# Optimization experiments

Hardware: AMD Instinct MI355X
Metric: run time of the kernel (lower is better)

The kernel has to match this reference:

```python
import jax, jax.numpy as jnp
import numpy as np

NUM_SLOTS = 50
NUM_TAGS = 1 + 2 * NUM_SLOTS  # 'O' + B-/I- per slot = 101
BATCH = 256
SEQ_LEN = 2048


def _build_type_indices():
    # Replicates CRF.build_transitions index construction for a BIO label vocab.
    labels = ['O'] + [p + f's{i}' for i in range(NUM_SLOTS) for p in ('B-', 'I-')]
    m1 = {'O': 0, 'B': 1, 'I': 2}
    m2 = {'O': 0, 'B': 3, 'I': 4}
    t0 = np.zeros((NUM_TAGS, NUM_TAGS), dtype=np.int64)
    t1 = np.zeros((NUM_TAGS, NUM_TAGS), dtype=np.int64)
    for i, li in enumerate(labels):
        for j, lj in enumerate(labels):
            if li != 'O' and li[2:] != lj[2:]:
                t0[i, j], t1[i, j] = m1[li[0]], m2[lj[0]]
            else:
                t0[i, j], t1[i, j] = m1[li[0]], m1[lj[0]]
    return jnp.asarray(t0), jnp.asarray(t1)


def setup_inputs() -> dict:
    key = jax.random.key(0)
    k1, k2, k3, k4, k5, k6 = jax.random.split(key, 6)
    feats = jax.random.normal(k1, (BATCH, SEQ_LEN, NUM_TAGS), dtype=jnp.float32)
    # cdt_transitions is log of the fixed prior table in the original module
    cdt = jnp.log(jnp.array([[0.6, 0.4, 0.001, 0.001, 0.001],
                             [0.3, 0.1, 0.1, 0.5, 0.001],
                             [0.6, 0.1, 0.1, 0.2, 0.001]], dtype=jnp.float32))
    start_transitions = jax.random.normal(k2, (NUM_TAGS,), dtype=jnp.float32)
    stop_transitions = jax.random.normal(k3, (NUM_TAGS,), dtype=jnp.float32)
    # random valid lengths in [S/2, S]; mask[:, :len] = 1
    lengths = jax.random.randint(k4, (BATCH,), SEQ_LEN // 2, SEQ_LEN + 1)
    mask = (jnp.arange(SEQ_LEN)[None, :] < lengths[:, None]).astype(jnp.int32)
    tags = jax.random.randint(k5, (BATCH, SEQ_LEN), 0, NUM_TAGS)
    types0, types1 = _build_type_indices()
    return {
        'feats': feats,
        'cdt_transitions': cdt,
        'start_transitions': start_transitions,
        'stop_transitions': stop_transitions,
        'mask': mask,
        'tags': tags,
        'types0': types0,
        'types1': types1,
    }


def reference(feats, cdt_transitions, start_transitions, stop_transitions,
              mask, tags, types0, types1):
    # build_transitions: gather (num_tags, num_tags) log-transition matrix
    trans = cdt_transitions[types0, types1]  # (T, T)
    B, S, T = feats.shape
    maskb = mask.astype(bool)

    # ---- forward algorithm (log partition) via lax.scan over time ----
    feats_t = jnp.swapaxes(feats, 0, 1)   # (S, B, T)
    mask_t = jnp.swapaxes(maskb, 0, 1)    # (S, B)
    partition0 = feats_t[0] + start_transitions[None, :]  # (B, T)

    def step(partition, xs):
        f, mk = xs  # f: (B, T), mk: (B,)
        # cur_values[b, i, j] = f[b, j] + partition[b, i] + trans[i, j]
        cur = f[:, None, :] + partition[:, :, None] + trans[None, :, :]
        cur_partition = jax.nn.logsumexp(cur, axis=1)  # (B, T)
        new_partition = jnp.where(mk[:, None], cur_partition, partition)
        return new_partition, None

    partition, _ = jax.lax.scan(step, partition0, (feats_t[1:], mask_t[1:]))
    forward_score = jax.nn.logsumexp(partition + stop_transitions[None, :], axis=1)  # (B,)

    # ---- gold path score ----
    mf = maskb.astype(feats.dtype)
    feat_score = jnp.sum(
        jnp.take_along_axis(feats, tags[..., None], axis=2)[..., 0] * mf, axis=1)
    trans_score = jnp.sum(trans[tags[:, :-1], tags[:, 1:]] * mf[:, 1:], axis=1)
    start_score = start_transitions[tags[:, 0]]
    lengths = jnp.sum(mask, axis=1).astype(jnp.int32)  # (B,)
    end_ids = jnp.take_along_axis(tags, (lengths - 1)[:, None], axis=1)[:, 0]
    stop_score = stop_transitions[end_ids]
    gold_score = feat_score + start_score + trans_score + stop_score

    return forward_score - gold_score  # (B,) negative log-likelihood per sequence
```

## Files before the change

kernel.cpp:

```cpp
#include <hip/hip_runtime.h>
#include <math.h>

#define NSLOTS 50
#define T 101
#define SEQ 2048
#define CHUNK 16

template<int CTRL>
__device__ __forceinline__ float dpp_xadd(float v) {
    int x = __builtin_amdgcn_update_dpp(0, __float_as_int(v), CTRL, 0xF, 0xF, true);
    return v + __int_as_float(x);
}

__device__ __forceinline__ float wsum64(float v) {
    v = dpp_xadd<0xB1>(v);
    v = dpp_xadd<0x4E>(v);
    v = dpp_xadd<0x141>(v);
    v = dpp_xadd<0x140>(v);
    v = dpp_xadd<0x142>(v);
    v = dpp_xadd<0x143>(v);
    int s = __builtin_amdgcn_readlane(__float_as_int(v), 63);
    return __int_as_float(s);
}

__device__ __forceinline__ void gl_lds(const float* g, float* lds) {
#if __has_builtin(__builtin_amdgcn_global_load_lds)
    __builtin_amdgcn_global_load_lds((const __attribute__((address_space(1))) void*)g,
        (__attribute__((address_space(3))) void*)lds, 4, 0, 0);
#else
    lds[threadIdx.x & 63] = *g;
#endif
}

__global__ __launch_bounds__(192, 1) void crf_nll_kernel(
    const float* __restrict__ feats,
    const float* __restrict__ cdt,
    const float* __restrict__ start_t,
    const float* __restrict__ stop_t,
    const int*   __restrict__ mask,
    const int*   __restrict__ tags,
    float*       __restrict__ out)
{
    const int b = blockIdx.x, tid = threadIdx.x;
    const int wave = tid >> 6, l = tid & 63;
    const float* fb = feats + (size_t)b * SEQ * T;
    const int*   mb = mask + (size_t)b * SEQ;
    const int*   tb = tags + (size_t)b * SEQ;

    __shared__ float S[64 * 128];
    __shared__ float res[2];

    float mc = 0.f;
    for (int t = l; t < SEQ; t += 64) mc += (float)mb[t];
    const int len    = (int)(wsum64(mc) + 0.5f);
    const int nsteps = len - 1;
    const int nper   = (nsteps + CHUNK - 1) / CHUNK;
    const int nfull  = nsteps / CHUNK;

    const float actm = (l < NSLOTS) ? 1.f : 0.f;
    const int aB = (2*l+1 <= 100) ? 2*l+1 : 100;
    const int aI = (2*l+2 <= 100) ? 2*l+2 : 100;
    const int s1 = (2*l+1 <= 100) ? 2*l+1 : 0;
    const int s2 = (2*l+2 <= 100) ? 2*l+2 : 0;

    const float pOO=__expf(cdt[0]),  pOB=__expf(cdt[1]),  pOI=__expf(cdt[2]);
    const float pBO=__expf(cdt[5]),  pBBs=__expf(cdt[6]), pBIs=__expf(cdt[7]),
                pBBd=__expf(cdt[8]), pBId=__expf(cdt[9]);
    const float pIO=__expf(cdt[10]), pIBs=__expf(cdt[11]), pIIs=__expf(cdt[12]),
                pIBd=__expf(cdt[13]), pIId=__expf(cdt[14]);
    const float dBB=pBBs-pBBd, dIB=pIBs-pIBd, dBI=pBIs-pBId, dII=pIIs-pIId;

    float xB=0.f, xI=0.f, xO=1.f, accF=0.f, uB=0.f, uI=0.f, pOOxO=pOO;
    int accE = 0;
    float f0B=0,f0I=0,f0O=0,f1B=0,f1I=0,f1O=0;
    float gs = 0.f;

    if (wave == 1) {
        #pragma unroll
        for (int k = 0; k < 2*CHUNK; ++k) {
            const float* row = fb + (size_t)(1 + k) * T;
            float* dst = &S[(size_t)k * 128];
            gl_lds(row + s1, dst);
            gl_lds(row + s2, dst + 64);
        }
    } else if (wave == 0) {
        float pO0 = fb[0] + start_t[0];
        xB = actm * __expf(fb[aB] + start_t[aB] - pO0);
        xI = actm * __expf(fb[aI] + start_t[aI] - pO0);
        accF = pO0;
        uB = __builtin_fmaf(xB, dBB, __builtin_fmaf(xI, dIB, pOB));
        uI = __builtin_fmaf(xB, dBI, __builtin_fmaf(xI, dII, pOI));
    } else {
        if (l == 0) {
            int tg0 = tb[0];
            gs = fb[tg0] + start_t[tg0];
        }
    }
    __syncthreads();

    if (wave == 0) {
        f0B = S[l];       f0I = S[64 + l];       f0O = S[50];
        f1B = S[128 + l]; f1I = S[128 + 64 + l]; f1O = S[128 + 50];
    }

#define STEP_BODY(GUARDED)                                                     \
    {                                                                          \
        const int t  = 1 + p * CHUNK + k;                                      \
        const int w2 = ((t + 1) & 63) << 7;              \
        float nB = S[w2 + l], nI = S[w2 + 64 + l], nO = S[w2 + 50];            \
        if (!(GUARDED) || t <= nsteps) {                                       \
            float gB = actm * __expf(f0B - f0O);                \
            float gI = actm * __expf(f0I - f0O);                               \
            int   ke = ((__float_as_int(xO) >> 23) & 0xFF) - 127;              \
            float r  = __int_as_float((127 - ke) << 23);     \
            accE += ke;                                                        \
            float XB = wsum64(xB);                                             \
            float XI = wsum64(xI);                                             \
            float NOr = __builtin_fmaf(XI,pIO, __builtin_fmaf(XB,pBO, pOOxO));  \
            float NB  = gB * __builtin_fmaf(XI,pIBd, __builtin_fmaf(XB,pBBd, uB)); \
            float NI  = gI * __builtin_fmaf(XI,pIId, __builtin_fmaf(XB,pBId, uI)); \
            xB = NB * r; xI = NI * r; xO = NOr * r;                            \
            pOOxO = pOO * xO;                          \
            uB = __builtin_fmaf(xB, dBB, __builtin_fmaf(xI, dIB, pOB * xO));   \
            uI = __builtin_fmaf(xB, dBI, __builtin_fmaf(xI, dII, pOI * xO));   \
            accF += f0O;                                                       \
        }                                                                      \
        f0B=f1B; f0I=f1I; f0O=f1O; f1B=nB; f1I=nI; f1O=nO;                     \
    }

    for (int p = 0; p < nper; ++p) {
        if (wave == 0) {
            if (p < nfull) {
                #pragma unroll
                for (int k = 0; k < CHUNK; ++k) STEP_BODY(false)
            } else {
                #pragma unroll
                for (int k = 0; k < CHUNK; ++k) STEP_BODY(true)
            }
        } else if (wave == 1) {
            const int ci = p + 2;
            #pragma unroll
            for (int k = 0; k < CHUNK; ++k) {
                int t = 1 + ci * CHUNK + k;
                t = (t < SEQ) ? t : (SEQ - 1);
                const float* row = fb + (size_t)t * T;
                float* dst = &S[(size_t)((ci * CHUNK + k) & 63) * 128];
                gl_lds(row + s1, dst);
                gl_lds(row + s2, dst + 64);
            }
        } else {
            if (p >= 1 && l < CHUNK) {
                int t = 1 + (p - 1) * CHUNK + l;
                if (t <= nsteps) {
                    int tg = tb[t], tp = tb[t - 1];
                    int c1 = (tp == 0) ? 0 : ((tp & 1) ? 1 : 2);
                    int c2 = (tg == 0) ? 0 : ((tg & 1) ? 1 : 2);
                    int si = (tp - 1) >> 1, sj = (tg - 1) >> 1;
                    int t1 = (tp != 0 && si != sj) ? ((c2 == 0) ? 0 : c2 + 2) : c2;
                    gs += cdt[c1 * 5 + t1];
                    int idx = (tg == 0) ? 50 : ((tg & 1) ? ((tg - 1) >> 1) : (64 + ((tg - 2) >> 1)));
                    gs += S[(((t - 1) & 63) << 7) + idx];
                }
            }
        }
        __syncthreads();
    }
#undef STEP_BODY

    if (wave == 0) {
        float W = actm * (xB * __expf(stop_t[aB]) + xI * __expf(stop_t[aI]));
        float tot = wsum64(W) + xO * __expf(stop_t[0]);
        float fwd = accF + 0.69314718055994530942f * (float)accE + __logf(tot);
        if (l == 0) res[0] = fwd;
    } else if (wave == 2) {
        if (l < CHUNK) {
            int t = 1 + (nper - 1) * CHUNK + l;
            if (t >= 1 && t <= nsteps) {
                int tg = tb[t], tp = tb[t - 1];
                int c1 = (tp == 0) ? 0 : ((tp & 1) ? 1 : 2);
                int c2 = (tg == 0) ? 0 : ((tg & 1) ? 1 : 2);
                int si = (tp - 1) >> 1, sj = (tg - 1) >> 1;
                int t1 = (tp != 0 && si != sj) ? ((c2 == 0) ? 0 : c2 + 2) : c2;
                gs += cdt[c1 * 5 + t1];
                int idx = (tg == 0) ? 50 : ((tg & 1) ? ((tg - 1) >> 1) : (64 + ((tg - 2) >> 1)));
                gs += S[(((t - 1) & 63) << 7) + idx];
            }
        }
        float gold = wsum64(gs);
        if (l == 0) res[1] = gold + stop_t[tb[len - 1]];
    }
    __syncthreads();
    if (tid == 0) out[b] = res[0] - res[1];
}

extern "C" void kernel_launch(void* const* d_in, const int* in_sizes, int n_in,
                              void* d_out, int out_size, void* d_ws, size_t ws_size,
                              hipStream_t stream) {
    const float* feats   = (const float*)d_in[0];
    const float* cdt     = (const float*)d_in[1];
    const float* start_t = (const float*)d_in[2];
    const float* stop_t  = (const float*)d_in[3];
    const int*   mask    = (const int*)d_in[4];
    const int*   tags    = (const int*)d_in[5];
    float* out = (float*)d_out;

    crf_nll_kernel<<<256, 192, 0, stream>>>(feats, cdt, start_t, stop_t, mask, tags, out);
}
```

Before: 246.7 us.

## Restructure CRF forward recurrence to break the wave-reduction dependency chain

Reformulates the per-step scaled forward recurrence so the next step's slot sums (XB, XI) come from precomputed reductions (GB, SB, GI, SI) of gate and correction terms instead of a wave reduction on the freshly computed state. The wave reductions can then overlap with the scalar state update rather than sitting on the serial critical path of each timestep. In exchange each step does four cross-lane reductions instead of two, the rescaling is applied one step late with a final exponent correction, and the reordered float arithmetic may change rounding.

```diff
diff --git a/kernel.cpp b/kernel.cpp
--- a/kernel.cpp
+++ b/kernel.cpp
@@ -70,9 +70,17 @@
                 pIBd=__expf(cdt[13]), pIId=__expf(cdt[14]);
     const float dBB=pBBs-pBBd, dIB=pIBs-pIBd, dBI=pBIs-pBId, dII=pIIs-pIId;
 
-    float xB=0.f, xI=0.f, xO=1.f, accF=0.f, uB=0.f, uI=0.f, pOOxO=pOO;
-    int accE = 0;
-    float f0B=0,f0I=0,f0O=0,f1B=0,f1I=0,f1O=0;
+    float xB=0.f, xI=0.f, xO=1.f;
+    float XB=0.f, XI=0.f;
+    float SB=0.f, SI=0.f;
+    float GB=0.f, GI=0.f;
+    float fB_=0.f, fI_=0.f;
+    float gfB=0.f, gfI=0.f;
+    float zB=0.f, zI=0.f;
+    float egB=0.f, egI=0.f;
+    float rr=1.f;
+    float accF=0.f; int accE=0;
+    float fOa=0.f, fOb=0.f;
     float gs = 0.f;
 
     if (wave == 1) {
@@ -83,49 +91,77 @@
             gl_lds(row + s1, dst);
             gl_lds(row + s2, dst + 64);
         }
-    } else if (wave == 0) {
+    } else if (wave == 2) {
+        if (l == 0) { int tg0 = tb[0]; gs = fb[tg0] + start_t[tg0]; }
+    } else {
         float pO0 = fb[0] + start_t[0];
         xB = actm * __expf(fb[aB] + start_t[aB] - pO0);
         xI = actm * __expf(fb[aI] + start_t[aI] - pO0);
         accF = pO0;
-        uB = __builtin_fmaf(xB, dBB, __builtin_fmaf(xI, dIB, pOB));
-        uI = __builtin_fmaf(xB, dBI, __builtin_fmaf(xI, dII, pOI));
-    } else {
-        if (l == 0) {
-            int tg0 = tb[0];
-            gs = fb[tg0] + start_t[tg0];
-        }
+        XB = wsum64(xB); XI = wsum64(xI);
     }
     __syncthreads();
 
     if (wave == 0) {
-        f0B = S[l];       f0I = S[64 + l];       f0O = S[50];
-        f1B = S[128 + l]; f1I = S[128 + 64 + l]; f1O = S[128 + 50];
+        float eB0 = __builtin_fmaf(pIBd, XI, pBBd * XB);
+        float eI0 = __builtin_fmaf(pIId, XI, pBId * XB);
+        fB_ = pOB + eB0;
+        fI_ = pOI + eI0;
+        float F1B = S[l],       F1I = S[64 + l],       F1O = S[50];
+        float F2B = S[128 + l], F2I = S[128 + 64 + l], F2O = S[128 + 50];
+        float egB1 = __expf(F1B - F1O), egI1 = __expf(F1I - F1O);
+        float mgB1 = actm * egB1, mgI1 = actm * egI1;
+        GB = wsum64(mgB1); GI = wsum64(mgI1);
+        gfB = mgB1 * fB_;  gfI = mgI1 * fI_;
+        float tB = __builtin_fmaf(dIB, xI, dBB * xB);
+        float tI = __builtin_fmaf(dII, xI, dBI * xB);
+        zB = egB1 * tB;  zI = egI1 * tI;
+        SB = wsum64(zB); SI = wsum64(zI);
+        egB = __expf(F2B - F2O); egI = __expf(F2I - F2O);
+        fOa = F1O; fOb = F2O; rr = 1.f;
     }
 
 #define STEP_BODY(GUARDED)                                                     \
     {                                                                          \
         const int t  = 1 + p * CHUNK + k;                                      \
         const int w2 = ((t + 1) & 63) << 7;              \
-        float nB = S[w2 + l], nI = S[w2 + 64 + l], nO = S[w2 + 50];            \
+        float nB_ = S[w2 + l], nI_ = S[w2 + 64 + l], nO_ = S[w2 + 50];         \
         if (!(GUARDED) || t <= nsteps) {                                       \
-            float gB = actm * __expf(f0B - f0O);                \
-            float gI = actm * __expf(f0I - f0O);                               \
-            int   ke = ((__float_as_int(xO) >> 23) & 0xFF) - 127;              \
-            float r  = __int_as_float((127 - ke) << 23);     \
+                                                      \
+            xB = __builtin_fmaf(rr, zB, gfB);                                  \
+            xI = __builtin_fmaf(rr, zI, gfI);                                  \
+                             \
+            float xOn = rr * __builtin_fmaf(pIO, XI,                           \
+                              __builtin_fmaf(pBO, XB, pOO * xO));              \
+            float XBn = rr * __builtin_fmaf(GB, fB_, SB);                      \
+            float XIn = rr * __builtin_fmaf(GI, fI_, SI);                      \
+            accF += fOa;                                                       \
+                                                         \
+            float eBn = __builtin_fmaf(pIBd, XIn, pBBd * XBn);                 \
+            float eIn = __builtin_fmaf(pIId, XIn, pBId * XBn);                 \
+            fB_ = __builtin_fmaf(pOB, xOn, eBn);                               \
+            fI_ = __builtin_fmaf(pOI, xOn, eIn);                               \
+                                   \
+            int ke = ((__float_as_int(xOn) >> 23) & 0xFF) - 127;               \
             accE += ke;                                                        \
-            float XB = wsum64(xB);                                             \
-            float XI = wsum64(xI);                                             \
-            float NOr = __builtin_fmaf(XI,pIO, __builtin_fmaf(XB,pBO, pOOxO));  \
-            float NB  = gB * __builtin_fmaf(XI,pIBd, __builtin_fmaf(XB,pBBd, uB)); \
-            float NI  = gI * __builtin_fmaf(XI,pIId, __builtin_fmaf(XB,pBId, uI)); \
-            xB = NB * r; xI = NI * r; xO = NOr * r;                            \
-            pOOxO = pOO * xO;                          \
-            uB = __builtin_fmaf(xB, dBB, __builtin_fmaf(xI, dIB, pOB * xO));   \
-            uI = __builtin_fmaf(xB, dBI, __builtin_fmaf(xI, dII, pOI * xO));   \
-            accF += f0O;                                                       \
+            float rn = __int_as_float((127 - ke) << 23);                       \
+                                         \
+            float mgB = actm * egB, mgI = actm * egI;                          \
+            gfB = (rn * mgB) * fB_;  gfI = (rn * mgI) * fI_;                   \
+                                     \
+            float tB = __builtin_fmaf(dIB, xI, dBB * xB);                      \
+            float tI = __builtin_fmaf(dII, xI, dBI * xB);                      \
+            float zBn = egB * tB, zIn = egI * tI;                              \
+            SB = wsum64(zBn); SI = wsum64(zIn);                                \
+            zB = zBn; zI = zIn;                                                \
+                                                              \
+            GB = wsum64(mgB); GI = wsum64(mgI);                                \
+                                           \
+            egB = __expf(nB_ - nO_); egI = __expf(nI_ - nO_);                  \
+                                                                   \
+            xO = xOn; XB = XBn; XI = XIn; rr = rn;                             \
         }                                                                      \
-        f0B=f1B; f0I=f1I; f0O=f1O; f1B=nB; f1I=nI; f1O=nO;                     \
+        fOa = fOb; fOb = nO_;                                                  \
     }
 
     for (int p = 0; p < nper; ++p) {
@@ -168,6 +204,8 @@
 #undef STEP_BODY
 
     if (wave == 0) {
+        int keF = ((__float_as_int(xO) >> 23) & 0xFF) - 127;
+        accE -= keF;
         float W = actm * (xB * __expf(stop_t[aB]) + xI * __expf(stop_t[aI]));
         float tot = wsum64(W) + xO * __expf(stop_t[0]);
         float fwd = accF + 0.69314718055994530942f * (float)accE + __logf(tot);
```

Result: slower. 312.2 us (+26.5%).

## Process two sequences per block with interleaved recurrences for ILP

Applied to the files above, without the earlier changes.

Each workgroup now handles two batch elements, interleaving their forward recurrences, gold-score work and LDS prefetch so the two independent dependency chains can overlap latency within one wave. Grid size halves from 256 to 128 blocks. The goal is to hide the serial latency of the DPP wave reductions and exponentials in the scan. In exchange, each block runs as long as the longer of its two sequences, half the CUs may sit idle, and register and LDS use double.

```diff
diff --git a/kernel.cpp b/kernel.cpp
--- a/kernel.cpp
+++ b/kernel.cpp
@@ -41,21 +41,29 @@
     const int*   __restrict__ tags,
     float*       __restrict__ out)
 {
-    const int b = blockIdx.x, tid = threadIdx.x;
+    const int bid = blockIdx.x, tid = threadIdx.x;
     const int wave = tid >> 6, l = tid & 63;
-    const float* fb = feats + (size_t)b * SEQ * T;
-    const int*   mb = mask + (size_t)b * SEQ;
-    const int*   tb = tags + (size_t)b * SEQ;
-
-    __shared__ float S[64 * 128];
-    __shared__ float res[2];
-
-    float mc = 0.f;
-    for (int t = l; t < SEQ; t += 64) mc += (float)mb[t];
-    const int len    = (int)(wsum64(mc) + 0.5f);
-    const int nsteps = len - 1;
-    const int nper   = (nsteps + CHUNK - 1) / CHUNK;
-    const int nfull  = nsteps / CHUNK;
+    const int b0 = 2 * bid, b1 = 2 * bid + 1;
+    const float* fbA = feats + (size_t)b0 * SEQ * T;
+    const float* fbB = feats + (size_t)b1 * SEQ * T;
+    const int* mbA = mask + (size_t)b0 * SEQ;
+    const int* mbB = mask + (size_t)b1 * SEQ;
+    const int* tbA = tags + (size_t)b0 * SEQ;
+    const int* tbB = tags + (size_t)b1 * SEQ;
+
+    __shared__ float LA[64 * 128];
+    __shared__ float LB[64 * 128];
+    __shared__ float res[4];
+
+    float mca = 0.f, mcb = 0.f;
+    for (int t = l; t < SEQ; t += 64) { mca += (float)mbA[t]; mcb += (float)mbB[t]; }
+    const int lenA = (int)(wsum64(mca) + 0.5f);
+    const int lenB = (int)(wsum64(mcb) + 0.5f);
+    const int nsA = lenA - 1, nsB = lenB - 1;
+    const int nsMin = (nsA < nsB) ? nsA : nsB;
+    const int nperA = (nsA + CHUNK - 1) / CHUNK, nperB = (nsB + CHUNK - 1) / CHUNK;
+    const int nper  = (nperA > nperB) ? nperA : nperB;
+    const int nfullzip = ((nsA < nsB ? nsA : nsB)) / CHUNK;
 
     const float actm = (l < NSLOTS) ? 1.f : 0.f;
     const int aB = (2*l+1 <= 100) ? 2*l+1 : 100;
@@ -70,127 +78,188 @@
                 pIBd=__expf(cdt[13]), pIId=__expf(cdt[14]);
     const float dBB=pBBs-pBBd, dIB=pIBs-pIBd, dBI=pBIs-pBId, dII=pIIs-pIId;
 
-    float xB=0.f, xI=0.f, xO=1.f, accF=0.f, uB=0.f, uI=0.f, pOOxO=pOO;
-    int accE = 0;
-    float f0B=0,f0I=0,f0O=0,f1B=0,f1I=0,f1O=0;
-    float gs = 0.f;
+    float xaB=0.f, xaI=0.f, xaO=1.f, uaB=0.f, uaI=0.f, pOOxOa=pOO, accFa=0.f;
+    float xbB=0.f, xbI=0.f, xbO=1.f, ubB=0.f, ubI=0.f, pOOxOb=pOO, accFb=0.f;
+    int accEa=0, accEb=0;
+    float f0aB=0,f0aI=0,f0aO=0,f1aB=0,f1aI=0,f1aO=0;
+    float f0bB=0,f0bI=0,f0bO=0,f1bB=0,f1bI=0,f1bO=0;
+    float gsA=0.f, gsB=0.f;
+
+    auto step_one = [&](float f0B, float f0I, float f0O,
+                        float& xB, float& xI, float& xO,
+                        float& uB, float& uI, float& pOOxO,
+                        float& accF, int& accE) {
+        float gB = actm * __expf(f0B - f0O);
+        float gI = actm * __expf(f0I - f0O);
+        int   ke = ((__float_as_int(xO) >> 23) & 0xFF) - 127;
+        float r  = __int_as_float((127 - ke) << 23);
+        accE += ke;
+        float XB = wsum64(xB);
+        float XI = wsum64(xI);
+        float NO = __builtin_fmaf(XI,pIO, __builtin_fmaf(XB,pBO, pOOxO));
+        float NB = gB * __builtin_fmaf(XI,pIBd, __builtin_fmaf(XB,pBBd, uB));
+        float NI = gI * __builtin_fmaf(XI,pIId, __builtin_fmaf(XB,pBId, uI));
+        xB = NB * r; xI = NI * r; xO = NO * r;
+        pOOxO = pOO * xO;
+        uB = __builtin_fmaf(xB, dBB, __builtin_fmaf(xI, dIB, pOB * xO));
+        uI = __builtin_fmaf(xB, dBI, __builtin_fmaf(xI, dII, pOI * xO));
+        accF += f0O;
+    };
+
+    auto gold_term = [&](const int* tbX, const float* LX, int t) -> float {
+        int tg = tbX[t], tp = tbX[t - 1];
+        int c1 = (tp == 0) ? 0 : ((tp & 1) ? 1 : 2);
+        int c2 = (tg == 0) ? 0 : ((tg & 1) ? 1 : 2);
+        int si = (tp - 1) >> 1, sj = (tg - 1) >> 1;
+        int t1 = (tp != 0 && si != sj) ? ((c2 == 0) ? 0 : c2 + 2) : c2;
+        float v = cdt[c1 * 5 + t1];
+        int idx = (tg == 0) ? 50 : ((tg & 1) ? ((tg - 1) >> 1) : (64 + ((tg - 2) >> 1)));
+        v += LX[(((t - 1) & 63) << 7) + idx];
+        return v;
+    };
 
     if (wave == 1) {
         #pragma unroll
         for (int k = 0; k < 2*CHUNK; ++k) {
-            const float* row = fb + (size_t)(1 + k) * T;
-            float* dst = &S[(size_t)k * 128];
-            gl_lds(row + s1, dst);
-            gl_lds(row + s2, dst + 64);
-        }
-    } else if (wave == 0) {
-        float pO0 = fb[0] + start_t[0];
-        xB = actm * __expf(fb[aB] + start_t[aB] - pO0);
-        xI = actm * __expf(fb[aI] + start_t[aI] - pO0);
-        accF = pO0;
-        uB = __builtin_fmaf(xB, dBB, __builtin_fmaf(xI, dIB, pOB));
-        uI = __builtin_fmaf(xB, dBI, __builtin_fmaf(xI, dII, pOI));
+            const float* rowA = fbA + (size_t)(1 + k) * T;
+            const float* rowB = fbB + (size_t)(1 + k) * T;
+            float* dA = &LA[(size_t)k * 128];
+            float* dB = &LB[(size_t)k * 128];
+            gl_lds(rowA + s1, dA);       gl_lds(rowB + s1, dB);
+            gl_lds(rowA + s2, dA + 64);  gl_lds(rowB + s2, dB + 64);
+        }
+    } else if (wave == 2) {
+        if (l == 0) {
+            int tg0 = tbA[0]; gsA = fbA[tg0] + start_t[tg0];
+            int th0 = tbB[0]; gsB = fbB[th0] + start_t[th0];
+        }
     } else {
-        if (l == 0) {
-            int tg0 = tb[0];
-            gs = fb[tg0] + start_t[tg0];
-        }
+        float pO0a = fbA[0] + start_t[0];
+        float pO0b = fbB[0] + start_t[0];
+        xaB = actm * __expf(fbA[aB] + start_t[aB] - pO0a);
+        xbB = actm * __expf(fbB[aB] + start_t[aB] - pO0b);
+        xaI = actm * __expf(fbA[aI] + start_t[aI] - pO0a);
+        xbI = actm * __expf(fbB[aI] + start_t[aI] - pO0b);
+        accFa = pO0a; accFb = pO0b;
+        uaB = __builtin_fmaf(xaB, dBB, __builtin_fmaf(xaI, dIB, pOB));
+        ubB = __builtin_fmaf(xbB, dBB, __builtin_fmaf(xbI, dIB, pOB));
+        uaI = __builtin_fmaf(xaB, dBI, __builtin_fmaf(xaI, dII, pOI));
+        ubI = __builtin_fmaf(xbB, dBI, __builtin_fmaf(xbI, dII, pOI));
     }
     __syncthreads();
 
     if (wave == 0) {
-        f0B = S[l];       f0I = S[64 + l];       f0O = S[50];
-        f1B = S[128 + l]; f1I = S[128 + 64 + l]; f1O = S[128 + 50];
-    }
-
-#define STEP_BODY(GUARDED)                                                     \
+        f0aB = LA[l];       f0aI = LA[64 + l];       f0aO = LA[50];
+        f0bB = LB[l];       f0bI = LB[64 + l];       f0bO = LB[50];
+        f1aB = LA[128 + l]; f1aI = LA[128 + 64 + l]; f1aO = LA[128 + 50];
+        f1bB = LB[128 + l]; f1bI = LB[128 + 64 + l]; f1bO = LB[128 + 50];
+    }
+
+#define STEP_ZIP(CHECKED)                                                      \
     {                                                                          \
         const int t  = 1 + p * CHUNK + k;                                      \
-        const int w2 = ((t + 1) & 63) << 7;              \
-        float nB = S[w2 + l], nI = S[w2 + 64 + l], nO = S[w2 + 50];            \
-        if (!(GUARDED) || t <= nsteps) {                                       \
-            float gB = actm * __expf(f0B - f0O);                \
-            float gI = actm * __expf(f0I - f0O);                               \
-            int   ke = ((__float_as_int(xO) >> 23) & 0xFF) - 127;              \
-            float r  = __int_as_float((127 - ke) << 23);     \
-            accE += ke;                                                        \
-            float XB = wsum64(xB);                                             \
-            float XI = wsum64(xI);                                             \
-            float NOr = __builtin_fmaf(XI,pIO, __builtin_fmaf(XB,pBO, pOOxO));  \
-            float NB  = gB * __builtin_fmaf(XI,pIBd, __builtin_fmaf(XB,pBBd, uB)); \
-            float NI  = gI * __builtin_fmaf(XI,pIId, __builtin_fmaf(XB,pBId, uI)); \
-            xB = NB * r; xI = NI * r; xO = NOr * r;                            \
-            pOOxO = pOO * xO;                          \
-            uB = __builtin_fmaf(xB, dBB, __builtin_fmaf(xI, dIB, pOB * xO));   \
-            uI = __builtin_fmaf(xB, dBI, __builtin_fmaf(xI, dII, pOI * xO));   \
-            accF += f0O;                                                       \
+        const int w2 = ((t + 1) & 63) << 7;                                    \
+        float naB = LA[w2 + l],      nbB = LB[w2 + l];                         \
+        float naI = LA[w2 + 64 + l], nbI = LB[w2 + 64 + l];                    \
+        float naO = LA[w2 + 50],     nbO = LB[w2 + 50];                        \
+        if (!(CHECKED) || t <= nsMin) {                                        \
+            float gaB = actm * __expf(f0aB - f0aO);                            \
+            float gbB = actm * __expf(f0bB - f0bO);                            \
+            float gaI = actm * __expf(f0aI - f0aO);                            \
+            float gbI = actm * __expf(f0bI - f0bO);                            \
+            int kea = ((__float_as_int(xaO) >> 23) & 0xFF) - 127;              \
+            int keb = ((__float_as_int(xbO) >> 23) & 0xFF) - 127;              \
+            float ra = __int_as_float((127 - kea) << 23);                      \
+            float rb = __int_as_float((127 - keb) << 23);                      \
+            accEa += kea; accEb += keb;                                        \
+            float XaB = wsum64(xaB);                                           \
+            float XbB = wsum64(xbB);                                           \
+            float XaI = wsum64(xaI);                                           \
+            float XbI = wsum64(xbI);                                           \
+            float NaO = __builtin_fmaf(XaI,pIO, __builtin_fmaf(XaB,pBO, pOOxOa)); \
+            float NbO = __builtin_fmaf(XbI,pIO, __builtin_fmaf(XbB,pBO, pOOxOb)); \
+            float NaB = gaB * __builtin_fmaf(XaI,pIBd, __builtin_fmaf(XaB,pBBd, uaB)); \
+            float NbB = gbB * __builtin_fmaf(XbI,pIBd, __builtin_fmaf(XbB,pBBd, ubB)); \
+            float NaI = gaI * __builtin_fmaf(XaI,pIId, __builtin_fmaf(XaB,pBId, uaI)); \
+            float NbI = gbI * __builtin_fmaf(XbI,pIId, __builtin_fmaf(XbB,pBId, ubI)); \
+            xaB = NaB * ra;  xbB = NbB * rb;                                   \
+            xaI = NaI * ra;  xbI = NbI * rb;                                   \
+            xaO = NaO * ra;  xbO = NbO * rb;                                   \
+            pOOxOa = pOO * xaO;  pOOxOb = pOO * xbO;                           \
+            uaB = __builtin_fmaf(xaB, dBB, __builtin_fmaf(xaI, dIB, pOB * xaO)); \
+            ubB = __builtin_fmaf(xbB, dBB, __builtin_fmaf(xbI, dIB, pOB * xbO)); \
+            uaI = __builtin_fmaf(xaB, dBI, __builtin_fmaf(xaI, dII, pOI * xaO)); \
+            ubI = __builtin_fmaf(xbB, dBI, __builtin_fmaf(xbI, dII, pOI * xbO)); \
+            accFa += f0aO; accFb += f0bO;                                      \
+        } else {                                                               \
+            if (t <= nsA) step_one(f0aB,f0aI,f0aO, xaB,xaI,xaO,                \
+                                   uaB,uaI,pOOxOa, accFa,accEa);               \
+            if (t <= nsB) step_one(f0bB,f0bI,f0bO, xbB,xbI,xbO,                \
+                                   ubB,ubI,pOOxOb, accFb,accEb);               \
         }                                                                      \
-        f0B=f1B; f0I=f1I; f0O=f1O; f1B=nB; f1I=nI; f1O=nO;                     \
+        f0aB=f1aB; f0aI=f1aI; f0aO=f1aO; f1aB=naB; f1aI=naI; f1aO=naO;         \
+        f0bB=f1bB; f0bI=f1bI; f0bO=f1bO; f1bB=nbB; f1bI=nbI; f1bO=nbO;         \
     }
 
     for (int p = 0; p < nper; ++p) {
         if (wave == 0) {
-            if (p < nfull) {
+            if (p < nfullzip) {
                 #pragma unroll
-                for (int k = 0; k < CHUNK; ++k) STEP_BODY(false)
+                for (int k = 0; k < CHUNK; ++k) STEP_ZIP(false)
             } else {
                 #pragma unroll
-                for (int k = 0; k < CHUNK; ++k) STEP_BODY(true)
+                for (int k = 0; k < CHUNK; ++k) STEP_ZIP(true)
             }
         } else if (wave == 1) {
             const int ci = p + 2;
             #pragma unroll
             for (int k = 0; k < CHUNK; ++k) {
-                int t = 1 + ci * CHUNK + k;
-                t = (t < SEQ) ? t : (SEQ - 1);
-                const float* row = fb + (size_t)t * T;
-                float* dst = &S[(size_t)((ci * CHUNK + k) & 63) * 128];
-                gl_lds(row + s1, dst);
-                gl_lds(row + s2, dst + 64);
+                int tt = 1 + ci * CHUNK + k;
+                int tc = (tt < SEQ) ? tt : (SEQ - 1);
+                const float* rowA = fbA + (size_t)tc * T;
+                const float* rowB = fbB + (size_t)tc * T;
+                float* dA = &LA[(size_t)((ci * CHUNK + k) & 63) * 128];
+                float* dB = &LB[(size_t)((ci * CHUNK + k) & 63) * 128];
+                gl_lds(rowA + s1, dA);       gl_lds(rowB + s1, dB);
+                gl_lds(rowA + s2, dA + 64);  gl_lds(rowB + s2, dB + 64);
             }
         } else {
             if (p >= 1 && l < CHUNK) {
                 int t = 1 + (p - 1) * CHUNK + l;
-                if (t <= nsteps) {
-                    int tg = tb[t], tp = tb[t - 1];
-                    int c1 = (tp == 0) ? 0 : ((tp & 1) ? 1 : 2);
-                    int c2 = (tg == 0) ? 0 : ((tg & 1) ? 1 : 2);
-                    int si = (tp - 1) >> 1, sj = (tg - 1) >> 1;
-                    int t1 = (tp != 0 && si != sj) ? ((c2 == 0) ? 0 : c2 + 2) : c2;
-                    gs += cdt[c1 * 5 + t1];
-                    int idx = (tg == 0) ? 50 : ((tg & 1) ? ((tg - 1) >> 1) : (64 + ((tg - 2) >> 1)));
-                    gs += S[(((t - 1) & 63) << 7) + idx];
-                }
+                if (t <= nsA) gsA += gold_term(tbA, LA, t);
+                if (t <= nsB) gsB += gold_term(tbB, LB, t);
             }
         }
         __syncthreads();
     }
-#undef STEP_BODY
+#undef STEP_ZIP
 
     if (wave == 0) {
-        float W = actm * (xB * __expf(stop_t[aB]) + xI * __expf(stop_t[aI]));
-        float tot = wsum64(W) + xO * __expf(stop_t[0]);
-        float fwd = accF + 0.69314718055994530942f * (float)accE + __logf(tot);
-        if (l == 0) res[0] = fwd;
+        float Wa = actm * (xaB * __expf(stop_t[aB]) + xaI * __expf(stop_t[aI]));
+        float Wb = actm * (xbB * __expf(stop_t[aB]) + xbI * __expf(stop_t[aI]));
+        float totA = wsum64(Wa) + xaO * __expf(stop_t[0]);
+        float totB = wsum64(Wb) + xbO * __expf(stop_t[0]);
+        float fwdA = accFa + 0.69314718055994530942f * (float)accEa + __logf(totA);
+        float fwdB = accFb + 0.69314718055994530942f * (float)accEb + __logf(totB);
+        if (l == 0) { res[0] = fwdA; res[2] = fwdB; }
     } else if (wave == 2) {
         if (l < CHUNK) {
             int t = 1 + (nper - 1) * CHUNK + l;
-            if (t >= 1 && t <= nsteps) {
-                int tg = tb[t], tp = tb[t - 1];
-                int c1 = (tp == 0) ? 0 : ((tp & 1) ? 1 : 2);
-                int c2 = (tg == 0) ? 0 : ((tg & 1) ? 1 : 2);
-                int si = (tp - 1) >> 1, sj = (tg - 1) >> 1;
-                int t1 = (tp != 0 && si != sj) ? ((c2 == 0) ? 0 : c2 + 2) : c2;
-                gs += cdt[c1 * 5 + t1];
-                int idx = (tg == 0) ? 50 : ((tg & 1) ? ((tg - 1) >> 1) : (64 + ((tg - 2) >> 1)));
-                gs += S[(((t - 1) & 63) << 7) + idx];
-            }
-        }
-        float gold = wsum64(gs);
-        if (l == 0) res[1] = gold + stop_t[tb[len - 1]];
+            if (t >= 1 && t <= nsA) gsA += gold_term(tbA, LA, t);
+            if (t >= 1 && t <= nsB) gsB += gold_term(tbB, LB, t);
+        }
+        float goldA = wsum64(gsA);
+        float goldB = wsum64(gsB);
+        if (l == 0) {
+            res[1] = goldA + stop_t[tbA[lenA - 1]];
+            res[3] = goldB + stop_t[tbB[lenB - 1]];
+        }
     }
     __syncthreads();
-    if (tid == 0) out[b] = res[0] - res[1];
+    if (tid == 0) {
+        out[b0] = res[0] - res[1];
+        out[b1] = res[2] - res[3];
+    }
 }
 
 extern "C" void kernel_launch(void* const* d_in, const int* in_sizes, int n_in,
@@ -204,5 +273,5 @@
     const int*   tags    = (const int*)d_in[5];
     float* out = (float*)d_out;
 
-    crf_nll_kernel<<<256, 192, 0, stream>>>(feats, cdt, start_t, stop_t, mask, tags, out);
-}
+    crf_nll_kernel<<<128, 192, 0, stream>>>(feats, cdt, start_t, stop_t, mask, tags, out);
+}
```

New measurement: 405.8 us. 1.65x slower.

## Precompute per-step emission sums in helper wave and split recurrence reductions

Applied to the files above, without the earlier changes.

Wave 2 now precomputes the per-step wave sums of the exponentiated B/I emissions for the next chunk and stores them in a double-buffered LDS array. The serial recurrence on wave 0 is rewritten algebraically so that only the transition-dependent part needs a fresh cross-lane reduction each step. That reduction's DPP stages are interleaved with the LDS prefetch for the next row and pipelined one step ahead. The aim is to shorten the serial dependency chain per timestep, at the cost of more registers, an extra LDS buffer and more work on the helper wave.

```diff
diff --git a/kernel.cpp b/kernel.cpp
--- a/kernel.cpp
+++ b/kernel.cpp
@@ -21,6 +21,10 @@
     v = dpp_xadd<0x143>(v);
     int s = __builtin_amdgcn_readlane(__float_as_int(v), 63);
     return __int_as_float(s);
+}
+
+__device__ __forceinline__ float rdl63(float v) {
+    return __int_as_float(__builtin_amdgcn_readlane(__float_as_int(v), 63));
 }
 
 __device__ __forceinline__ void gl_lds(const float* g, float* lds) {
@@ -48,6 +52,7 @@
     const int*   tb = tags + (size_t)b * SEQ;
 
     __shared__ float S[64 * 128];
+    __shared__ float2 Gbuf[2][17];
     __shared__ float res[2];
 
     float mc = 0.f;
@@ -70,10 +75,48 @@
                 pIBd=__expf(cdt[13]), pIId=__expf(cdt[14]);
     const float dBB=pBBs-pBBd, dIB=pIBs-pIBd, dBI=pBIs-pBId, dII=pIIs-pIId;
 
-    float xB=0.f, xI=0.f, xO=1.f, accF=0.f, uB=0.f, uI=0.f, pOOxO=pOO;
-    int accE = 0;
-    float f0B=0,f0I=0,f0O=0,f1B=0,f1I=0,f1O=0;
+    float xB=0.f, xI=0.f, xO=1.f;
+    float XBp=0.f, XIp=0.f;
+    float phBp=0.f, phIp=0.f;
+    float pOOx=pOO;
+    float rr=1.f; int keC=0;
+    float zB=0.f, zI=0.f;
+    float gBc=0.f, gIc=0.f;
+    float raB=0.f, raI=0.f;
+    float fOc=0.f;
+    float accF=0.f; int accE=0;
+    float f0B=0,f0I=0,f0O=0, f1B=0,f1I=0,f1O=0, f2B=0,f2I=0,f2O=0, f3B=0,f3I=0,f3O=0;
+    int w3 = 0;
     float gs = 0.f;
+
+    auto do_G = [&](int chunkIdx) {
+        const int par = chunkIdx & 1;
+        const int tbase = 1 + chunkIdx * CHUNK;
+        #pragma unroll
+        for (int kk = 0; kk < CHUNK; kk += 4) {
+            const float* r0 = &S[(size_t)((tbase + kk + 0 - 1) & 63) << 7];
+            const float* r1 = &S[(size_t)((tbase + kk + 1 - 1) & 63) << 7];
+            const float* r2 = &S[(size_t)((tbase + kk + 2 - 1) & 63) << 7];
+            const float* r3 = &S[(size_t)((tbase + kk + 3 - 1) & 63) << 7];
+            float o0 = r0[50], o1 = r1[50], o2 = r2[50], o3 = r3[50];
+            float g0 = actm*__expf(r0[l]-o0), h0 = actm*__expf(r0[64+l]-o0);
+            float g1 = actm*__expf(r1[l]-o1), h1 = actm*__expf(r1[64+l]-o1);
+            float g2 = actm*__expf(r2[l]-o2), h2 = actm*__expf(r2[64+l]-o2);
+            float g3 = actm*__expf(r3[l]-o3), h3 = actm*__expf(r3[64+l]-o3);
+#define GSTAGE(C) g0=dpp_xadd<C>(g0); h0=dpp_xadd<C>(h0); g1=dpp_xadd<C>(g1); h1=dpp_xadd<C>(h1); \
+                  g2=dpp_xadd<C>(g2); h2=dpp_xadd<C>(h2); g3=dpp_xadd<C>(g3); h3=dpp_xadd<C>(h3);
+            GSTAGE(0xB1) GSTAGE(0x4E) GSTAGE(0x141) GSTAGE(0x140) GSTAGE(0x142) GSTAGE(0x143)
+#undef GSTAGE
+            float G0=rdl63(g0), H0=rdl63(h0), G1=rdl63(g1), H1=rdl63(h1);
+            float G2=rdl63(g2), H2=rdl63(h2), G3=rdl63(g3), H3=rdl63(h3);
+            if (l == 0) {
+                Gbuf[par][kk+0] = make_float2(G0,H0);
+                Gbuf[par][kk+1] = make_float2(G1,H1);
+                Gbuf[par][kk+2] = make_float2(G2,H2);
+                Gbuf[par][kk+3] = make_float2(G3,H3);
+            }
+        }
+    };
 
     if (wave == 1) {
         #pragma unroll
@@ -88,54 +131,132 @@
         xB = actm * __expf(fb[aB] + start_t[aB] - pO0);
         xI = actm * __expf(fb[aI] + start_t[aI] - pO0);
         accF = pO0;
-        uB = __builtin_fmaf(xB, dBB, __builtin_fmaf(xI, dIB, pOB));
-        uI = __builtin_fmaf(xB, dBI, __builtin_fmaf(xI, dII, pOI));
     } else {
-        if (l == 0) {
-            int tg0 = tb[0];
-            gs = fb[tg0] + start_t[tg0];
-        }
+        if (l == 0) { int tg0 = tb[0]; gs = fb[tg0] + start_t[tg0]; }
     }
     __syncthreads();
 
     if (wave == 0) {
-        f0B = S[l];       f0I = S[64 + l];       f0O = S[50];
-        f1B = S[128 + l]; f1I = S[128 + 64 + l]; f1O = S[128 + 50];
-    }
-
-#define STEP_BODY(GUARDED)                                                     \
+        XBp = wsum64(xB); XIp = wsum64(xI);
+        phBp = __builtin_fmaf(pIBd, XIp, __builtin_fmaf(pBBd, XBp, pOB));
+        phIp = __builtin_fmaf(pIId, XIp, __builtin_fmaf(pBId, XBp, pOI));
+        pOOx = pOO; xO = 1.f;
+        float r1B=S[l], r1I=S[64+l], r1O=S[50];
+        f3B=S[128+l]; f3I=S[128+64+l]; f3O=S[128+50];
+        f0B=S[256+l]; f0I=S[256+64+l]; f0O=S[256+50];
+        gBc = actm * __expf(r1B - r1O);
+        gIc = actm * __expf(r1I - r1O);
+        fOc = r1O;
+        float tB0 = __builtin_fmaf(dIB, xI, dBB * xB);
+        float tI0 = __builtin_fmaf(dII, xI, dBI * xB);
+        zB = gBc * tB0; zI = gIc * tI0;
+        raB = dpp_xadd<0xB1>(zB);  raI = dpp_xadd<0xB1>(zI);
+        raB = dpp_xadd<0x4E>(raB); raI = dpp_xadd<0x4E>(raI);
+        raB = dpp_xadd<0x141>(raB);raI = dpp_xadd<0x141>(raI);
+        raB = dpp_xadd<0x140>(raB);raI = dpp_xadd<0x140>(raI);
+        raB = dpp_xadd<0x142>(raB);raI = dpp_xadd<0x142>(raI);
+        raB = dpp_xadd<0x143>(raB);raI = dpp_xadd<0x143>(raI);
+        rr = 1.f; keC = 0; w3 = 256;
+    } else if (wave == 2) {
+        do_G(0);
+    }
+    __syncthreads();
+
+#define PHASE(K, cB_,cI_,cO_, nB_,nI_,nO_, Gu_,Gv_)                            \
     {                                                                          \
-        const int t  = 1 + p * CHUNK + k;                                      \
-        const int w2 = ((t + 1) & 63) << 7;              \
-        float nB = S[w2 + l], nI = S[w2 + 64 + l], nO = S[w2 + 50];            \
-        if (!(GUARDED) || t <= nsteps) {                                       \
-            float gB = actm * __expf(f0B - f0O);                \
-            float gI = actm * __expf(f0I - f0O);                               \
-            int   ke = ((__float_as_int(xO) >> 23) & 0xFF) - 127;              \
-            float r  = __int_as_float((127 - ke) << 23);     \
-            accE += ke;                                                        \
-            float XB = wsum64(xB);                                             \
-            float XI = wsum64(xI);                                             \
-            float NOr = __builtin_fmaf(XI,pIO, __builtin_fmaf(XB,pBO, pOOxO));  \
-            float NB  = gB * __builtin_fmaf(XI,pIBd, __builtin_fmaf(XB,pBBd, uB)); \
-            float NI  = gI * __builtin_fmaf(XI,pIId, __builtin_fmaf(XB,pBId, uI)); \
-            xB = NB * r; xI = NI * r; xO = NOr * r;                            \
-            pOOxO = pOO * xO;                          \
-            uB = __builtin_fmaf(xB, dBB, __builtin_fmaf(xI, dIB, pOB * xO));   \
-            uI = __builtin_fmaf(xB, dBI, __builtin_fmaf(xI, dII, pOI * xO));   \
-            accF += f0O;                                                       \
-        }                                                                      \
-        f0B=f1B; f0I=f1I; f0O=f1O; f1B=nB; f1I=nI; f1O=nO;                     \
+        float xBn = __builtin_fmaf(gBc, phBp, zB) * rr;                        \
+        float xIn = __builtin_fmaf(gIc, phIp, zI) * rr;                        \
+        float eBt = __expf(cB_ - cO_);                                         \
+        float eIt = __expf(cI_ - cO_);                                         \
+        float tBv = __builtin_fmaf(dIB, xIn, dBB * xBn);                       \
+        float tIv = __builtin_fmaf(dII, xIn, dBI * xBn);                       \
+        float gBn = actm * eBt;                                                \
+        float gIn = actm * eIt;                                                \
+        float zBn = gBn * tBv;                                                 \
+        float zIn = gIn * tIv;                                                 \
+        float qB = dpp_xadd<0xB1>(zBn);                                        \
+        float qI = dpp_xadd<0xB1>(zIn);                                        \
+        w3 = (w3 + 128) & 8191;                                                \
+        nB_ = S[w3 + l];                                                       \
+        qB = dpp_xadd<0x4E>(qB);                                               \
+        qI = dpp_xadd<0x4E>(qI);                                               \
+        nI_ = S[w3 + 64 + l];                                                  \
+        qB = dpp_xadd<0x141>(qB);                                              \
+        qI = dpp_xadd<0x141>(qI);                                              \
+        nO_ = S[w3 + 50];                                                      \
+        qB = dpp_xadd<0x140>(qB);                                              \
+        qI = dpp_xadd<0x140>(qI);                                              \
+        Gv_ = Gr[(K) + 1];                                                     \
+        qB = dpp_xadd<0x142>(qB);                                              \
+        qI = dpp_xadd<0x142>(qI);                                              \
+        accF += fOc;                                                           \
+        accE += keC;                                                           \
+        qB = dpp_xadd<0x143>(qB);                                              \
+        qI = dpp_xadd<0x143>(qI);                                              \
+        __builtin_amdgcn_sched_barrier(0);                                     \
+        float SBr = rdl63(raB);                                                \
+        float SIr = rdl63(raI);                                                \
+        float XBn = __builtin_fmaf(Gu_.x, phBp, SBr) * rr;                     \
+        float XIn = __builtin_fmaf(Gu_.y, phIp, SIr) * rr;                     \
+        float xOn = rr * __builtin_fmaf(pIO, XIp, __builtin_fmaf(pBO, XBp, pOOx)); \
+        float pOBx = pOB * xOn;                                                \
+        float pOIx = pOI * xOn;                                                \
+        pOOx = pOO * xOn;                                                      \
+        float phBn = __builtin_fmaf(pIBd, XIn, __builtin_fmaf(pBBd, XBn, pOBx)); \
+        float phIn = __builtin_fmaf(pIId, XIn, __builtin_fmaf(pBId, XBn, pOIx)); \
+        int ike = ((__float_as_int(xOn) >> 23) & 0xFF) - 127;                  \
+        rr = __int_as_float((127 - ike) << 23);                                \
+        keC = ike;                                                             \
+        xB = xBn; xI = xIn; zB = zBn; zI = zIn;                                \
+        gBc = gBn; gIc = gIn; raB = qB; raI = qI;                              \
+        XBp = XBn; XIp = XIn; xO = xOn;                                        \
+        phBp = phBn; phIp = phIn; fOc = cO_;                                   \
     }
 
     for (int p = 0; p < nper; ++p) {
         if (wave == 0) {
             if (p < nfull) {
-                #pragma unroll
-                for (int k = 0; k < CHUNK; ++k) STEP_BODY(false)
+                const float2* Gr = &Gbuf[p & 1][0];
+                float2 rGa = Gr[0];
+                float2 rGb = rGa;
+                PHASE(0,  f3B,f3I,f3O, f1B,f1I,f1O, rGa, rGb)
+                PHASE(1,  f0B,f0I,f0O, f2B,f2I,f2O, rGb, rGa)
+                PHASE(2,  f1B,f1I,f1O, f3B,f3I,f3O, rGa, rGb)
+                PHASE(3,  f2B,f2I,f2O, f0B,f0I,f0O, rGb, rGa)
+                PHASE(4,  f3B,f3I,f3O, f1B,f1I,f1O, rGa, rGb)
+                PHASE(5,  f0B,f0I,f0O, f2B,f2I,f2O, rGb, rGa)
+                PHASE(6,  f1B,f1I,f1O, f3B,f3I,f3O, rGa, rGb)
+                PHASE(7,  f2B,f2I,f2O, f0B,f0I,f0O, rGb, rGa)
+                PHASE(8,  f3B,f3I,f3O, f1B,f1I,f1O, rGa, rGb)
+                PHASE(9,  f0B,f0I,f0O, f2B,f2I,f2O, rGb, rGa)
+                PHASE(10, f1B,f1I,f1O, f3B,f3I,f3O, rGa, rGb)
+                PHASE(11, f2B,f2I,f2O, f0B,f0I,f0O, rGb, rGa)
+                PHASE(12, f3B,f3I,f3O, f1B,f1I,f1O, rGa, rGb)
+                PHASE(13, f0B,f0I,f0O, f2B,f2I,f2O, rGb, rGa)
+                PHASE(14, f1B,f1I,f1O, f3B,f3I,f3O, rGa, rGb)
+                PHASE(15, f2B,f2I,f2O, f0B,f0I,f0O, rGb, rGa)
             } else {
-                #pragma unroll
-                for (int k = 0; k < CHUNK; ++k) STEP_BODY(true)
+                for (int k = 0; k < CHUNK; ++k) {
+                    int t = 1 + p * CHUNK + k;
+                    if (t <= nsteps) {
+                        const float* row = &S[(size_t)(((t - 1) & 63)) << 7];
+                        float fBv = row[l], fIv = row[64 + l], fOv = row[50];
+                        float gB = actm * __expf(fBv - fOv);
+                        float gI = actm * __expf(fIv - fOv);
+                        float pOBx = pOB * xO, pOIx = pOI * xO, pOOx2 = pOO * xO;
+                        float uB = __builtin_fmaf(xB, dBB, __builtin_fmaf(xI, dIB, pOBx));
+                        float uI = __builtin_fmaf(xB, dBI, __builtin_fmaf(xI, dII, pOIx));
+                        int   ke  = ((__float_as_int(xO) >> 23) & 0xFF) - 127;
+                        float rsc = __int_as_float((127 - ke) << 23);
+                        accE += ke; accF += fOv;
+                        float XBt = wsum64(xB);
+                        float XIt = wsum64(xI);
+                        float NO = __builtin_fmaf(XIt, pIO, __builtin_fmaf(XBt, pBO, pOOx2));
+                        float NB = gB * __builtin_fmaf(XIt, pIBd, __builtin_fmaf(XBt, pBBd, uB));
+                        float NI = gI * __builtin_fmaf(XIt, pIId, __builtin_fmaf(XBt, pBId, uI));
+                        xB = NB * rsc; xI = NI * rsc; xO = NO * rsc;
+                    }
+                }
             }
         } else if (wave == 1) {
             const int ci = p + 2;
@@ -149,6 +270,7 @@
                 gl_lds(row + s2, dst + 64);
             }
         } else {
+            do_G(p + 1);
             if (p >= 1 && l < CHUNK) {
                 int t = 1 + (p - 1) * CHUNK + l;
                 if (t <= nsteps) {
@@ -165,7 +287,7 @@
         }
         __syncthreads();
     }
-#undef STEP_BODY
+#undef PHASE
 
     if (wave == 0) {
         float W = actm * (xB * __expf(stop_t[aB]) + xI * __expf(stop_t[aI]));
```

After: 274.2 us. 1.11x slower.
